# Kernel optimization log

Measured on AMD Instinct MI355X. Metric: run time of the kernel, lower is better.

## Reference

```python
import jax, jax.numpy as jnp
import numpy as np

HIDDEN = 256
ATOM_DIM = 133
BOND_DIM = 14
MOL_DIM = 200
N_ATOMS = 120000
N_BONDS = 240000
MAX_DEG = 6
N_MOL = 4096
DEPTH = 3
EPS = 1e-5
NEG_SLOPE = 0.01


def _leaky(x):
    return jnp.where(x >= 0, x, NEG_SLOPE * x)


def _bn(x, w, b):
    # BatchNorm1d in training mode: batch mean / biased batch variance
    mu = jnp.mean(x, axis=0)
    var = jnp.var(x, axis=0)
    return (x - mu) * jax.lax.rsqrt(var + EPS) * w + b


def setup_inputs() -> dict:
    key = jax.random.key(0)
    ks = jax.random.split(key, 12)
    s = 0.02
    return {
        "atom_features": jax.random.normal(ks[0], (N_ATOMS, ATOM_DIM), jnp.float32),
        "bond_features": jax.random.normal(ks[1], (N_BONDS, BOND_DIM), jnp.float32),
        "bond_index": jax.random.randint(ks[2], (2, N_BONDS), 0, N_ATOMS, jnp.int32),
        "molecule_features": jax.random.normal(ks[3], (N_MOL, MOL_DIM), jnp.float32),
        # 1-based bond ids; 0 means padding (maps to prepended zero row)
        "atom_incoming_bond_map": jax.random.randint(ks[4], (N_ATOMS, MAX_DEG), 0, N_BONDS + 1, jnp.int32),
        "bond_reverse_map": jax.random.randint(ks[5], (N_BONDS,), 0, N_BONDS, jnp.int32),
        "atom_to_mol": jnp.sort(jax.random.randint(ks[6], (N_ATOMS,), 0, N_MOL, jnp.int32)),
        "W_i_w": jax.random.normal(ks[7], (HIDDEN, ATOM_DIM + BOND_DIM), jnp.float32) * s,
        "W_i_b": jnp.zeros((HIDDEN,), jnp.float32),
        "W_m_w": jax.random.normal(ks[8], (HIDDEN, HIDDEN), jnp.float32) * s,
        "W_m_b": jnp.zeros((HIDDEN,), jnp.float32),
        "W_a_w": jax.random.normal(ks[9], (HIDDEN, ATOM_DIM + HIDDEN), jnp.float32) * s,
        "W_a_b": jnp.zeros((HIDDEN,), jnp.float32),
        "bn_w": jnp.ones((HIDDEN,), jnp.float32),
        "bn_b": jnp.zeros((HIDDEN,), jnp.float32),
    }


def _atom_incoming_sum(h, aibm):
    # padded_h[0] is the zero row; aibm holds 1-based bond indices (0 = pad)
    padded_h = jnp.concatenate([jnp.zeros((1, h.shape[1]), h.dtype), h], axis=0)
    return padded_h[aibm].sum(axis=1)  # [n_atoms, H]


def reference(atom_features, bond_features, bond_index, molecule_features,
              atom_incoming_bond_map, bond_reverse_map, atom_to_mol,
              W_i_w, W_i_b, W_m_w, W_m_b, W_a_w, W_a_b, bn_w, bn_b):
    src = bond_index[0]
    # initial bond hidden states
    x = jnp.concatenate([bond_features, atom_features[src]], axis=1)
    h0 = _bn(_leaky(x @ W_i_w.T + W_i_b), bn_w, bn_b)
    h = h0
    for _ in range(DEPTH):
        atom_sums = _atom_incoming_sum(h, atom_incoming_bond_map)
        # message for bond b (v->w): sum of incoming bonds at v minus reverse bond
        m = atom_sums[src] - h[bond_reverse_map]
        h = _bn(_leaky(h0 + m @ W_m_w.T + W_m_b), bn_w, bn_b)
        # dropout_prob = 0.0 -> identity
    # bond -> atom pooling (empty atoms yield the cached zero vector)
    m_v = _atom_incoming_sum(h, atom_incoming_bond_map)
    h_v = _bn(_leaky(jnp.concatenate([atom_features, m_v], axis=1) @ W_a_w.T + W_a_b), bn_w, bn_b)
    # atom -> molecule pooling
    h_mol = jax.ops.segment_sum(h_v, atom_to_mol, num_segments=molecule_features.shape[0])
    return jnp.concatenate([h_mol, molecule_features], axis=1)
```

## Files before the change

### kernel.cpp

```cpp
#include <hip/hip_runtime.h>
#include <hip/hip_bf16.h>
#include <stdint.h>

#define NBONDS 240000
#define NATOMS 120000
#define HID    256
#define ADIM   133
#define BDIM   14
#define MOLDIM 200
#define NMOL   4096
#define KI     160
#define KM     256
#define KA     416
#define OUTW   456
#define BN_EPS 1e-5f
#define SLOPE  0.01f

typedef unsigned short u16;
typedef unsigned int   u32;
typedef __attribute__((ext_vector_type(8))) short short8;
typedef __attribute__((ext_vector_type(4))) float f32x4;

__device__ __forceinline__ float bf2f(u16 b){
  u32 u = ((u32)b) << 16;
  return __builtin_bit_cast(float, u);
}
__device__ __forceinline__ u16 f2bf(float f){
  u32 u = __builtin_bit_cast(u32, f);
  u32 r = (u + 0x7FFFu + ((u >> 16) & 1u)) >> 16;
  return (u16)r;
}
__device__ __forceinline__ void gload16(const void* g, void* l){
  __builtin_amdgcn_global_load_lds((const __attribute__((address_space(1))) u32*)g,
                                   (__attribute__((address_space(3))) u32*)l, 16, 0, 0);
}
__device__ __forceinline__ float leaky(float v){ return v >= 0.f ? v : SLOPE*v; }

__global__ void zero_f(float* p, int n){
  int i = blockIdx.x*blockDim.x + threadIdx.x;
  if(i < n) p[i] = 0.f;
}
__global__ void diag_k(float* out, int n, float wsz){
  int i = blockIdx.x*blockDim.x + threadIdx.x;
  for(; i < n; i += gridDim.x*blockDim.x) out[i] = (i == 0) ? wsz : 0.f;
}

__global__ void cvt_weights(const float* wi, const float* wm, const float* wa,
                            u16* wib, u16* wmb, u16* wab){
  int idx = blockIdx.x*blockDim.x + threadIdx.x;
  const int T0 = 256*KI, T1 = T0 + 256*KM, T2 = T1 + 256*KA;
  for(; idx < T2; idx += gridDim.x*blockDim.x){
    if(idx < T0){
      int n = idx / KI, k = idx % KI;
      wib[idx] = f2bf(k < 147 ? wi[n*147+k] : 0.f);
    } else if(idx < T1){
      int j = idx - T0;
      wmb[j] = f2bf(wm[j]);
    } else {
      int j = idx - T1;
      int n = j / KA, k = j % KA;
      float v = 0.f;
      if(k < 256)      v = wa[n*389 + 133 + k];
      else if(k < 389) v = wa[n*389 + (k - 256)];
      wab[j] = f2bf(v);
    }
  }
}

__global__ void affine_k(const float* __restrict__ stats, float* __restrict__ aff,
                         float invN, const float* __restrict__ bnw, const float* __restrict__ bnb){
  int c = threadIdx.x;
  float mu  = stats[c] * invN;
  float var = stats[256+c]*invN - mu*mu;
  float rs  = rsqrtf(var + BN_EPS);
  float sc  = rs * bnw[c];
  aff[c]     = sc;
  aff[256+c] = bnb[c] - mu*sc;
}


__global__ __launch_bounds__(256) void gemm0_k(
    const float* __restrict__ bondf, const float* __restrict__ atomf,
    const int* __restrict__ bidx, const u16* __restrict__ wib,
    const float* __restrict__ bi_, u16* __restrict__ Hout,
    float* __restrict__ stats)
{
  __shared__ u16 lA[2][4][64][8];
  __shared__ u16 lB[2][4][256][8];
  __shared__ float sred[512];
  const int tid=threadIdx.x, wave=tid>>6, lane=tid&63;
  const int wm=wave>>1, wn=wave&1, l15=lane&15, l4=lane>>4;
  const int r=tid&63, c=tid>>6;
  const int row0=blockIdx.x*64, row=row0+r;
  const int src = bidx[row];

  f32x4 acc[2][8];
  #pragma unroll
  for(int i=0;i<2;i++)
    #pragma unroll
    for(int j=0;j<8;j++){ f32x4 z={0.f,0.f,0.f,0.f}; acc[i][j]=z; }

  auto stgB=[&](int buf,int ks){
    #pragma unroll
    for(int kc=0;kc<4;kc++)
      gload16(wib + (size_t)(wave*64+lane)*KI + ks*32 + kc*8, &lB[buf][kc][wave*64][0]);
  };
  auto stgA=[&](int buf,int ks){
    int k0 = ks*32 + c*8;
    short8 o;
    #pragma unroll
    for(int e=0;e<8;e++){
      int kg=k0+e; float x=0.f;
      if(kg<BDIM) x=bondf[row*BDIM+kg];
      else if(kg<BDIM+ADIM) x=atomf[(size_t)src*ADIM+kg-BDIM];
      o[e]=(short)f2bf(x);
    }
    *(short8*)&lA[buf][c][r][0]=o;
  };
  auto mm=[&](int cur){
    short8 af[2];
    #pragma unroll
    for(int mf=0;mf<2;mf++) af[mf]=*(const short8*)&lA[cur][l4][wm*32+mf*16+l15][0];
    #pragma unroll
    for(int nf=0;nf<8;nf++){
      short8 b8=*(const short8*)&lB[cur][l4][wn*128+nf*16+l15][0];
      #pragma unroll
      for(int mf=0;mf<2;mf++)
        acc[mf][nf]=__builtin_amdgcn_mfma_f32_16x16x32_bf16(af[mf],b8,acc[mf][nf],0,0,0);
    }
  };

  stgA(0,0); stgB(0,0);
  __syncthreads();
  #pragma unroll
  for(int ks=0;ks<5;ks++){
    int cur=ks&1;
    if(ks<4){ stgA(cur^1,ks+1); stgB(cur^1,ks+1); }
    mm(cur);
    __syncthreads();
  }
  sred[tid]=0.f; sred[256+tid]=0.f;
  __syncthreads();
  #pragma unroll
  for(int nf=0;nf<8;nf++){
    int col=wn*128+nf*16+l15;
    float bc=bi_[col], ps=0.f, pq=0.f;
    #pragma unroll
    for(int mf=0;mf<2;mf++)
      #pragma unroll
      for(int j=0;j<4;j++){
        int grow=row0+wm*32+mf*16+l4*4+j;
        float h=leaky(acc[mf][nf][j]+bc);
        Hout[(size_t)grow*HID+col]=f2bf(h);
        ps+=h; pq+=h*h;
      }
    atomicAdd(&sred[col],ps); atomicAdd(&sred[256+col],pq);
  }
  __syncthreads();
  atomicAdd(&stats[tid],sred[tid]); atomicAdd(&stats[256+tid],sred[256+tid]);
}

__global__ __launch_bounds__(256) void gemml_k(
    const float* __restrict__ bondf, const float* __restrict__ atomf,
    const int* __restrict__ bidx, const int* __restrict__ brm,
    const int* __restrict__ aibm, const u16* __restrict__ Hin,
    const u16* __restrict__ zrow, const u16* __restrict__ wmb,
    const float* __restrict__ bm_, const u16* __restrict__ wib,
    const float* __restrict__ bi_, const float* __restrict__ ain,
    const float* __restrict__ aff0, u16* __restrict__ Hout,
    float* __restrict__ stats)
{
  __shared__ u16 lA[2][4][64][8];
  __shared__ u16 lB[2][4][256][8];
  __shared__ float sred[512];
  const int tid=threadIdx.x, wave=tid>>6, lane=tid&63;
  const int wm=wave>>1, wn=wave&1, l15=lane&15, l4=lane>>4;
  const int r=tid&63, c=tid>>6;
  const int row0=blockIdx.x*64, row=row0+r;

  sred[tid]=ain[tid]; sred[256+tid]=ain[256+tid];

  const int src = bidx[row];
  const int rev = brm[row];
  const u16* gbase[7];
  int cnt=0;
  #pragma unroll
  for(int j=0;j<6;j++){
    int id = aibm[src*6+j];
    gbase[j] = (id>0) ? (Hin + (size_t)(id-1)*HID) : zrow;
    cnt += (id>0);
  }
  gbase[6] = Hin + (size_t)rev*HID;
  const float cntm1 = (float)(cnt-1);

  f32x4 acc[2][8];
  #pragma unroll
  for(int i=0;i<2;i++)
    #pragma unroll
    for(int j=0;j<8;j++){ f32x4 z={0.f,0.f,0.f,0.f}; acc[i][j]=z; }

  auto stgB=[&](int buf,int ks,const u16* W,int ldk){
    #pragma unroll
    for(int kc=0;kc<4;kc++)
      gload16(W + (size_t)(wave*64+lane)*ldk + ks*32 + kc*8, &lB[buf][kc][wave*64][0]);
  };
  auto stgA1=[&](int buf,int ks){
    int kofs = ks*32 + c*8;
    short8 v[7];
    #pragma unroll
    for(int j=0;j<7;j++) v[j]=*(const short8*)(gbase[j]+kofs);
    short8 o;
    #pragma unroll
    for(int e=0;e<8;e++){
      float s=0.f;
      #pragma unroll
      for(int j=0;j<6;j++) s+=bf2f((u16)v[j][e]);
      s-=bf2f((u16)v[6][e]);
      float mv = sred[kofs+e]*s + cntm1*sred[256+kofs+e];
      o[e]=(short)f2bf(mv);
    }
    *(short8*)&lA[buf][c][r][0]=o;
  };
  auto stgA0=[&](int buf,int ks){
    int k0 = ks*32 + c*8;
    short8 o;
    #pragma unroll
    for(int e=0;e<8;e++){
      int kg=k0+e; float x=0.f;
      if(kg<BDIM) x=bondf[row*BDIM+kg];
      else if(kg<BDIM+ADIM) x=atomf[(size_t)src*ADIM+kg-BDIM];
      o[e]=(short)f2bf(x);
    }
    *(short8*)&lA[buf][c][r][0]=o;
  };
  auto mm=[&](int cur){
    short8 af[2];
    #pragma unroll
    for(int mf=0;mf<2;mf++) af[mf]=*(const short8*)&lA[cur][l4][wm*32+mf*16+l15][0];
    #pragma unroll
    for(int nf=0;nf<8;nf++){
      short8 b8=*(const short8*)&lB[cur][l4][wn*128+nf*16+l15][0];
      #pragma unroll
      for(int mf=0;mf<2;mf++)
        acc[mf][nf]=__builtin_amdgcn_mfma_f32_16x16x32_bf16(af[mf],b8,acc[mf][nf],0,0,0);
    }
  };

  __syncthreads();
  stgA1(0,0); stgB(0,0,wmb,KM);
  __syncthreads();
  #pragma unroll
  for(int ks=0;ks<8;ks++){
    int cur=ks&1;
    if(ks<7){ stgA1(cur^1,ks+1); stgB(cur^1,ks+1,wmb,KM); }
    mm(cur);
    __syncthreads();
  }
  u32 p1[2][8][2];
  #pragma unroll
  for(int mf=0;mf<2;mf++)
    #pragma unroll
    for(int nf=0;nf<8;nf++){
      p1[mf][nf][0]=((u32)f2bf(acc[mf][nf][1])<<16)|f2bf(acc[mf][nf][0]);
      p1[mf][nf][1]=((u32)f2bf(acc[mf][nf][3])<<16)|f2bf(acc[mf][nf][2]);
      f32x4 z={0.f,0.f,0.f,0.f}; acc[mf][nf]=z;
    }

  stgA0(0,0); stgB(0,0,wib,KI);
  __syncthreads();
  #pragma unroll
  for(int ks=0;ks<5;ks++){
    int cur=ks&1;
    if(ks<4){ stgA0(cur^1,ks+1); stgB(cur^1,ks+1,wib,KI); }
    mm(cur);
    __syncthreads();
  }

  sred[tid]=0.f; sred[256+tid]=0.f;
  __syncthreads();
  #pragma unroll
  for(int nf=0;nf<8;nf++){
    int col=wn*128+nf*16+l15;
    float bic=bi_[col], bmc=bm_[col];
    float s0=aff0[col], t0=aff0[256+col];
    float ps=0.f,pq=0.f;
    #pragma unroll
    for(int mf=0;mf<2;mf++)
      #pragma unroll
      for(int j=0;j<4;j++){
        int grow=row0+wm*32+mf*16+l4*4+j;
        float v0 = leaky(acc[mf][nf][j]+bic);
        v0 = s0*v0 + t0;
        u32 pw = p1[mf][nf][j>>1];
        float u1 = bf2f((u16)((j&1) ? (pw>>16) : (pw&0xffff)));
        float h = leaky(v0 + u1 + bmc);
        Hout[(size_t)grow*HID+col]=f2bf(h);
        ps+=h; pq+=h*h;
      }
    atomicAdd(&sred[col],ps); atomicAdd(&sred[256+col],pq);
  }
  __syncthreads();
  atomicAdd(&stats[tid],sred[tid]); atomicAdd(&stats[256+tid],sred[256+tid]);
}

__global__ __launch_bounds__(256) void gemmf_k(
    const float* __restrict__ atomf, const int* __restrict__ aibm,
    const u16* __restrict__ Hin, const u16* __restrict__ zrow,
    const u16* __restrict__ wab, const float* __restrict__ ba_,
    const float* __restrict__ ain, u16* __restrict__ Hvout,
    float* __restrict__ stats)
{
  __shared__ u16 lA[2][4][64][8];
  __shared__ u16 lB[2][4][256][8];
  __shared__ float sred[512];
  const int tid=threadIdx.x, wave=tid>>6, lane=tid&63;
  const int wm=wave>>1, wn=wave&1, l15=lane&15, l4=lane>>4;
  const int r=tid&63, c=tid>>6;
  const int row0=blockIdx.x*64, row=row0+r;

  sred[tid]=ain[tid]; sred[256+tid]=ain[256+tid];

  const u16* gbase[6];
  int cnt=0;
  #pragma unroll
  for(int j=0;j<6;j++){
    int id = aibm[row*6+j];
    gbase[j] = (id>0) ? (Hin + (size_t)(id-1)*HID) : zrow;
    cnt += (id>0);
  }
  const float cntf = (float)cnt;

  f32x4 acc[2][8];
  #pragma unroll
  for(int i=0;i<2;i++)
    #pragma unroll
    for(int j=0;j<8;j++){ f32x4 z={0.f,0.f,0.f,0.f}; acc[i][j]=z; }

  auto stgB=[&](int buf,int ks){
    #pragma unroll
    for(int kc=0;kc<4;kc++)
      gload16(wab + (size_t)(wave*64+lane)*KA + ks*32 + kc*8, &lB[buf][kc][wave*64][0]);
  };
  auto stgA=[&](int buf,int ks){
    int k0 = ks*32 + c*8;
    short8 o;
    if(ks<8){
      short8 v[6];
      #pragma unroll
      for(int j=0;j<6;j++) v[j]=*(const short8*)(gbase[j]+k0);
      #pragma unroll
      for(int e=0;e<8;e++){
        float s=0.f;
        #pragma unroll
        for(int j=0;j<6;j++) s+=bf2f((u16)v[j][e]);
        float mv = sred[k0+e]*s + cntf*sred[256+k0+e];
        o[e]=(short)f2bf(mv);
      }
    } else {
      #pragma unroll
      for(int e=0;e<8;e++){
        int kg = k0 + e - 256;
        float x = (kg < ADIM) ? atomf[(size_t)row*ADIM + kg] : 0.f;
        o[e]=(short)f2bf(x);
      }
    }
    *(short8*)&lA[buf][c][r][0]=o;
  };
  auto mm=[&](int cur){
    short8 af[2];
    #pragma unroll
    for(int mf=0;mf<2;mf++) af[mf]=*(const short8*)&lA[cur][l4][wm*32+mf*16+l15][0];
    #pragma unroll
    for(int nf=0;nf<8;nf++){
      short8 b8=*(const short8*)&lB[cur][l4][wn*128+nf*16+l15][0];
      #pragma unroll
      for(int mf=0;mf<2;mf++)
        acc[mf][nf]=__builtin_amdgcn_mfma_f32_16x16x32_bf16(af[mf],b8,acc[mf][nf],0,0,0);
    }
  };

  __syncthreads();
  stgA(0,0); stgB(0,0);
  __syncthreads();
  #pragma unroll
  for(int ks=0;ks<13;ks++){
    int cur=ks&1;
    if(ks<12){ stgA(cur^1,ks+1); stgB(cur^1,ks+1); }
    mm(cur);
    __syncthreads();
  }
  sred[tid]=0.f; sred[256+tid]=0.f;
  __syncthreads();
  #pragma unroll
  for(int nf=0;nf<8;nf++){
    int col=wn*128+nf*16+l15;
    float bc=ba_[col], ps=0.f,pq=0.f;
    #pragma unroll
    for(int mf=0;mf<2;mf++)
      #pragma unroll
      for(int j=0;j<4;j++){
        int grow=row0+wm*32+mf*16+l4*4+j;
        float h=leaky(acc[mf][nf][j]+bc);
        Hvout[(size_t)grow*HID+col]=f2bf(h);
        ps+=h; pq+=h*h;
      }
    atomicAdd(&sred[col],ps); atomicAdd(&sred[256+col],pq);
  }
  __syncthreads();
  atomicAdd(&stats[tid],sred[tid]); atomicAdd(&stats[256+tid],sred[256+tid]);
}

__device__ __forceinline__ int lbound(const int* a, int n, int v){
  int lo = 0, hi = n;
  while(lo < hi){ int mid = (lo+hi) >> 1; if(a[mid] < v) lo = mid+1; else hi = mid; }
  return lo;
}

__global__ void pool_k(const u16* __restrict__ hv, const float* __restrict__ aff,
                       const int* __restrict__ a2m, const float* __restrict__ molf,
                       float* __restrict__ outp){
  int m = blockIdx.x;
  int t = threadIdx.x;
  int start = lbound(a2m, NATOMS, m);
  int end   = lbound(a2m, NATOMS, m+1);
  int rg = t >> 5, cg = t & 31;
  float s[8];
  #pragma unroll
  for(int j=0;j<8;j++) s[j] = 0.f;
  for(int a = start + rg; a < end; a += 8){
    short8 v = *(const short8*)(hv + (size_t)a*HID + cg*8);
    #pragma unroll
    for(int j=0;j<8;j++) s[j] += bf2f((u16)v[j]);
  }
  __shared__ float red[8][256];
  #pragma unroll
  for(int j=0;j<8;j++) red[rg][cg*8+j] = s[j];
  __syncthreads();
  if(t < 256){
    float S = 0.f;
    #pragma unroll
    for(int r=0;r<8;r++) S += red[r][t];
    float cnt = (float)(end - start);
    outp[(size_t)m*OUTW + t] = aff[t]*S + cnt*aff[256+t];
  }
  if(t < MOLDIM){
    outp[(size_t)m*OUTW + HID + t] = molf[(size_t)m*MOLDIM + t];
  }
}

extern "C" void kernel_launch(void* const* d_in, const int* in_sizes, int n_in,
                              void* d_out, int out_size, void* d_ws, size_t ws_size,
                              hipStream_t stream){
  const float* atomf = (const float*)d_in[0];
  const float* bondf = (const float*)d_in[1];
  const int*   bidx  = (const int*)  d_in[2];
  const float* molf  = (const float*)d_in[3];
  const int*   aibm  = (const int*)  d_in[4];
  const int*   brm   = (const int*)  d_in[5];
  const int*   a2m   = (const int*)  d_in[6];
  const float* wi    = (const float*)d_in[7];
  const float* bi    = (const float*)d_in[8];
  const float* wm    = (const float*)d_in[9];
  const float* bm    = (const float*)d_in[10];
  const float* wa    = (const float*)d_in[11];
  const float* ba    = (const float*)d_in[12];
  const float* bnw   = (const float*)d_in[13];
  const float* bnb   = (const float*)d_in[14];
  float* outp = (float*)d_out;

  char* wsp = (char*)d_ws;
  size_t off = 0;
  auto alloc = [&](size_t bytes)->void*{
    void* p = wsp + off; off += (bytes + 255) & ~(size_t)255; return p;
  };
  u16* HA   = (u16*)alloc((size_t)NBONDS*HID*2);
  u16* HB   = (u16*)alloc((size_t)NBONDS*HID*2);
  u16* wib  = (u16*)alloc((size_t)256*KI*2);
  u16* wmb  = (u16*)alloc((size_t)256*KM*2);
  u16* wab  = (u16*)alloc((size_t)256*KA*2);
  float* stats = (float*)alloc(5*512*sizeof(float));
  float* affn  = (float*)alloc(5*512*sizeof(float));
  float* zrowf = (float*)alloc(512);
  size_t need = off;

  if(ws_size < need){
    diag_k<<<1024, 256, 0, stream>>>(outp, out_size, (float)ws_size);
    return;
  }
  const u16* zrow = (const u16*)zrowf;

  zero_f<<<(5248+255)/256, 256, 0, stream>>>(stats, 5248);
  cvt_weights<<<416, 256, 0, stream>>>(wi, wm, wa, wib, wmb, wab);

  gemm0_k<<<NBONDS/64, 256, 0, stream>>>(bondf, atomf, bidx, wib, bi, HA, stats);
  affine_k<<<1, 256, 0, stream>>>(stats, affn, 1.f/NBONDS, bnw, bnb);

  for(int t=0; t<3; t++){
    const u16* Hin  = (t & 1) ? HB : HA;
    u16*       Hout = (t & 1) ? HA : HB;
    gemml_k<<<NBONDS/64, 256, 0, stream>>>(bondf, atomf, bidx, brm, aibm,
                                           Hin, zrow, wmb, bm, wib, bi,
                                           affn + t*512, affn, Hout,
                                           stats + (t+1)*512);
    affine_k<<<1, 256, 0, stream>>>(stats + (t+1)*512, affn + (t+1)*512,
                                    1.f/NBONDS, bnw, bnb);
  }

  gemmf_k<<<NATOMS/64, 256, 0, stream>>>(atomf, aibm, HB, zrow, wab, ba,
                                         affn + 3*512, HA, stats + 4*512);
  affine_k<<<1, 256, 0, stream>>>(stats + 4*512, affn + 4*512, 1.f/NATOMS, bnw, bnb);

  pool_k<<<NMOL, 256, 0, stream>>>(HA, affn + 4*512, a2m, molf, outp);
}
```

Baseline: 1.988 ms.

## Split message gather out of GEMM kernels into separate gather kernels

New measurement: 1.870 ms. 1.06x faster.

```diff
diff --git a/kernel.cpp b/kernel.cpp
--- a/kernel.cpp
+++ b/kernel.cpp
@@ -52,7 +52,10 @@
   for(; idx < T2; idx += gridDim.x*blockDim.x){
     if(idx < T0){
       int n = idx / KI, k = idx % KI;
-      wib[idx] = f2bf(k < 147 ? wi[n*147+k] : 0.f);
+      float v = 0.f;
+      if(k < 133)      v = wi[n*147 + 14 + k];
+      else if(k < 147) v = wi[n*147 + (k - 133)];
+      wib[idx] = f2bf(v);
     } else if(idx < T1){
       int j = idx - T0;
       wmb[j] = f2bf(wm[j]);
@@ -76,6 +79,75 @@
   float sc  = rs * bnw[c];
   aff[c]     = sc;
   aff[256+c] = bnb[c] - mu*sc;
+}
+
+__global__ __launch_bounds__(256) void msg_k(
+    const int* __restrict__ bidx, const int* __restrict__ brm,
+    const int* __restrict__ aibm, const u16* __restrict__ Hin,
+    const u16* __restrict__ zrow, const float* __restrict__ ain,
+    u16* __restrict__ Mout)
+{
+  int t = threadIdx.x;
+  int b = blockIdx.x*8 + (t>>5);
+  int lane = t & 31;
+  int src = bidx[b];
+  int rev = brm[b];
+  const u16* gb[7];
+  int cnt = 0;
+  #pragma unroll
+  for(int j=0;j<6;j++){
+    int id = aibm[src*6+j];
+    gb[j] = (id>0) ? (Hin + (size_t)(id-1)*HID) : zrow;
+    cnt += (id>0);
+  }
+  gb[6] = Hin + (size_t)rev*HID;
+  int c = lane*8;
+  short8 v[7];
+  #pragma unroll
+  for(int j=0;j<7;j++) v[j] = *(const short8*)(gb[j]+c);
+  float cm1 = (float)(cnt-1);
+  short8 o;
+  #pragma unroll
+  for(int e=0;e<8;e++){
+    float s = 0.f;
+    #pragma unroll
+    for(int j=0;j<6;j++) s += bf2f((u16)v[j][e]);
+    s -= bf2f((u16)v[6][e]);
+    o[e] = (short)f2bf(ain[c+e]*s + cm1*ain[256+c+e]);
+  }
+  *(short8*)(Mout + (size_t)b*HID + c) = o;
+}
+
+__global__ __launch_bounds__(256) void msgv_k(
+    const int* __restrict__ aibm, const u16* __restrict__ Hin,
+    const u16* __restrict__ zrow, const float* __restrict__ ain,
+    u16* __restrict__ Mv)
+{
+  int t = threadIdx.x;
+  int a = blockIdx.x*8 + (t>>5);
+  int lane = t & 31;
+  const u16* gb[6];
+  int cnt = 0;
+  #pragma unroll
+  for(int j=0;j<6;j++){
+    int id = aibm[a*6+j];
+    gb[j] = (id>0) ? (Hin + (size_t)(id-1)*HID) : zrow;
+    cnt += (id>0);
+  }
+  int c = lane*8;
+  short8 v[6];
+  #pragma unroll
+  for(int j=0;j<6;j++) v[j] = *(const short8*)(gb[j]+c);
+  float cf = (float)cnt;
+  short8 o;
+  #pragma unroll
+  for(int e=0;e<8;e++){
+    float s = 0.f;
+    #pragma unroll
+    for(int j=0;j<6;j++) s += bf2f((u16)v[j][e]);
+    o[e] = (short)f2bf(ain[c+e]*s + cf*ain[256+c+e]);
+  }
+  *(short8*)(Mv + (size_t)a*HID + c) = o;
 }
 
 
@@ -111,8 +183,8 @@
     #pragma unroll
     for(int e=0;e<8;e++){
       int kg=k0+e; float x=0.f;
-      if(kg<BDIM) x=bondf[row*BDIM+kg];
-      else if(kg<BDIM+ADIM) x=atomf[(size_t)src*ADIM+kg-BDIM];
+      if(kg<ADIM) x=atomf[(size_t)src*ADIM+kg];
+      else if(kg<ADIM+BDIM) x=bondf[(size_t)row*BDIM+kg-ADIM];
       o[e]=(short)f2bf(x);
     }
     *(short8*)&lA[buf][c][r][0]=o;
@@ -162,12 +234,118 @@
 
 __global__ __launch_bounds__(256) void gemml_k(
     const float* __restrict__ bondf, const float* __restrict__ atomf,
-    const int* __restrict__ bidx, const int* __restrict__ brm,
-    const int* __restrict__ aibm, const u16* __restrict__ Hin,
-    const u16* __restrict__ zrow, const u16* __restrict__ wmb,
-    const float* __restrict__ bm_, const u16* __restrict__ wib,
-    const float* __restrict__ bi_, const float* __restrict__ ain,
-    const float* __restrict__ aff0, u16* __restrict__ Hout,
+    const int* __restrict__ bidx, u16* __restrict__ Mh,
+    const u16* __restrict__ wmb, const float* __restrict__ bm_,
+    const u16* __restrict__ wib, const float* __restrict__ bi_,
+    const float* __restrict__ aff0, float* __restrict__ stats)
+{
+  __shared__ u16 lA[2][4][64][8];
+  __shared__ u16 lB[2][4][256][8];
+  __shared__ float sred[512];
+  const int tid=threadIdx.x, wave=tid>>6, lane=tid&63;
+  const int wm=wave>>1, wn=wave&1, l15=lane&15, l4=lane>>4;
+  const int r=tid&63, c=tid>>6;
+  const int row0=blockIdx.x*64, row=row0+r;
+  const int src = bidx[row];
+
+  f32x4 acc[2][8];
+  #pragma unroll
+  for(int i=0;i<2;i++)
+    #pragma unroll
+    for(int j=0;j<8;j++){ f32x4 z={0.f,0.f,0.f,0.f}; acc[i][j]=z; }
+
+  auto stgB=[&](int buf,int ks,const u16* W,int ldk){
+    #pragma unroll
+    for(int kc=0;kc<4;kc++)
+      gload16(W + (size_t)(wave*64+lane)*ldk + ks*32 + kc*8, &lB[buf][kc][wave*64][0]);
+  };
+  auto stgA1=[&](int buf,int ks){
+    gload16(Mh + (size_t)(row0+lane)*KM + ks*32 + wave*8, &lA[buf][wave][0][0]);
+  };
+  auto stgA0=[&](int buf,int ks){
+    int k0 = ks*32 + c*8;
+    short8 o;
+    #pragma unroll
+    for(int e=0;e<8;e++){
+      int kg=k0+e; float x=0.f;
+      if(kg<ADIM) x=atomf[(size_t)src*ADIM+kg];
+      else if(kg<ADIM+BDIM) x=bondf[(size_t)row*BDIM+kg-ADIM];
+      o[e]=(short)f2bf(x);
+    }
+    *(short8*)&lA[buf][c][r][0]=o;
+  };
+  auto mm=[&](int cur){
+    short8 af[2];
+    #pragma unroll
+    for(int mf=0;mf<2;mf++) af[mf]=*(const short8*)&lA[cur][l4][wm*32+mf*16+l15][0];
+    #pragma unroll
+    for(int nf=0;nf<8;nf++){
+      short8 b8=*(const short8*)&lB[cur][l4][wn*128+nf*16+l15][0];
+      #pragma unroll
+      for(int mf=0;mf<2;mf++)
+        acc[mf][nf]=__builtin_amdgcn_mfma_f32_16x16x32_bf16(af[mf],b8,acc[mf][nf],0,0,0);
+    }
+  };
+
+  stgA1(0,0); stgB(0,0,wmb,KM);
+  __syncthreads();
+  #pragma unroll
+  for(int ks=0;ks<8;ks++){
+    int cur=ks&1;
+    if(ks<7){ stgA1(cur^1,ks+1); stgB(cur^1,ks+1,wmb,KM); }
+    mm(cur);
+    __syncthreads();
+  }
+  u32 p1[2][8][2];
+  #pragma unroll
+  for(int mf=0;mf<2;mf++)
+    #pragma unroll
+    for(int nf=0;nf<8;nf++){
+      p1[mf][nf][0]=((u32)f2bf(acc[mf][nf][1])<<16)|f2bf(acc[mf][nf][0]);
+      p1[mf][nf][1]=((u32)f2bf(acc[mf][nf][3])<<16)|f2bf(acc[mf][nf][2]);
+      f32x4 z={0.f,0.f,0.f,0.f}; acc[mf][nf]=z;
+    }
+
+  stgA0(0,0); stgB(0,0,wib,KI);
+  __syncthreads();
+  #pragma unroll
+  for(int ks=0;ks<5;ks++){
+    int cur=ks&1;
+    if(ks<4){ stgA0(cur^1,ks+1); stgB(cur^1,ks+1,wib,KI); }
+    mm(cur);
+    __syncthreads();
+  }
+
+  sred[tid]=0.f; sred[256+tid]=0.f;
+  __syncthreads();
+  #pragma unroll
+  for(int nf=0;nf<8;nf++){
+    int col=wn*128+nf*16+l15;
+    float bic=bi_[col], bmc=bm_[col];
+    float s0=aff0[col], t0=aff0[256+col];
+    float ps=0.f,pq=0.f;
+    #pragma unroll
+    for(int mf=0;mf<2;mf++)
+      #pragma unroll
+      for(int j=0;j<4;j++){
+        int grow=row0+wm*32+mf*16+l4*4+j;
+        float v0 = leaky(acc[mf][nf][j]+bic);
+        v0 = s0*v0 + t0;
+        u32 pw = p1[mf][nf][j>>1];
+        float u1 = bf2f((u16)((j&1) ? (pw>>16) : (pw&0xffff)));
+        float h = leaky(v0 + u1 + bmc);
+        Mh[(size_t)grow*HID+col]=f2bf(h);
+        ps+=h; pq+=h*h;
+      }
+    atomicAdd(&sred[col],ps); atomicAdd(&sred[256+col],pq);
+  }
+  __syncthreads();
+  atomicAdd(&stats[tid],sred[tid]); atomicAdd(&stats[256+tid],sred[256+tid]);
+}
+
+__global__ __launch_bounds__(256) void gemmf_k(
+    const float* __restrict__ atomf, u16* __restrict__ Mv,
+    const u16* __restrict__ wab, const float* __restrict__ ba_,
     float* __restrict__ stats)
 {
   __shared__ u16 lA[2][4][64][8];
@@ -178,158 +356,6 @@
   const int r=tid&63, c=tid>>6;
   const int row0=blockIdx.x*64, row=row0+r;
 
-  sred[tid]=ain[tid]; sred[256+tid]=ain[256+tid];
-
-  const int src = bidx[row];
-  const int rev = brm[row];
-  const u16* gbase[7];
-  int cnt=0;
-  #pragma unroll
-  for(int j=0;j<6;j++){
-    int id = aibm[src*6+j];
-    gbase[j] = (id>0) ? (Hin + (size_t)(id-1)*HID) : zrow;
-    cnt += (id>0);
-  }
-  gbase[6] = Hin + (size_t)rev*HID;
-  const float cntm1 = (float)(cnt-1);
-
-  f32x4 acc[2][8];
-  #pragma unroll
-  for(int i=0;i<2;i++)
-    #pragma unroll
-    for(int j=0;j<8;j++){ f32x4 z={0.f,0.f,0.f,0.f}; acc[i][j]=z; }
-
-  auto stgB=[&](int buf,int ks,const u16* W,int ldk){
-    #pragma unroll
-    for(int kc=0;kc<4;kc++)
-      gload16(W + (size_t)(wave*64+lane)*ldk + ks*32 + kc*8, &lB[buf][kc][wave*64][0]);
-  };
-  auto stgA1=[&](int buf,int ks){
-    int kofs = ks*32 + c*8;
-    short8 v[7];
-    #pragma unroll
-    for(int j=0;j<7;j++) v[j]=*(const short8*)(gbase[j]+kofs);
-    short8 o;
-    #pragma unroll
-    for(int e=0;e<8;e++){
-      float s=0.f;
-      #pragma unroll
-      for(int j=0;j<6;j++) s+=bf2f((u16)v[j][e]);
-      s-=bf2f((u16)v[6][e]);
-      float mv = sred[kofs+e]*s + cntm1*sred[256+kofs+e];
-      o[e]=(short)f2bf(mv);
-    }
-    *(short8*)&lA[buf][c][r][0]=o;
-  };
-  auto stgA0=[&](int buf,int ks){
-    int k0 = ks*32 + c*8;
-    short8 o;
-    #pragma unroll
-    for(int e=0;e<8;e++){
-      int kg=k0+e; float x=0.f;
-      if(kg<BDIM) x=bondf[row*BDIM+kg];
-      else if(kg<BDIM+ADIM) x=atomf[(size_t)src*ADIM+kg-BDIM];
-      o[e]=(short)f2bf(x);
-    }
-    *(short8*)&lA[buf][c][r][0]=o;
-  };
-  auto mm=[&](int cur){
-    short8 af[2];
-    #pragma unroll
-    for(int mf=0;mf<2;mf++) af[mf]=*(const short8*)&lA[cur][l4][wm*32+mf*16+l15][0];
-    #pragma unroll
-    for(int nf=0;nf<8;nf++){
-      short8 b8=*(const short8*)&lB[cur][l4][wn*128+nf*16+l15][0];
-      #pragma unroll
-      for(int mf=0;mf<2;mf++)
-        acc[mf][nf]=__builtin_amdgcn_mfma_f32_16x16x32_bf16(af[mf],b8,acc[mf][nf],0,0,0);
-    }
-  };
-
-  __syncthreads();
-  stgA1(0,0); stgB(0,0,wmb,KM);
-  __syncthreads();
-  #pragma unroll
-  for(int ks=0;ks<8;ks++){
-    int cur=ks&1;
-    if(ks<7){ stgA1(cur^1,ks+1); stgB(cur^1,ks+1,wmb,KM); }
-    mm(cur);
-    __syncthreads();
-  }
-  u32 p1[2][8][2];
-  #pragma unroll
-  for(int mf=0;mf<2;mf++)
-    #pragma unroll
-    for(int nf=0;nf<8;nf++){
-      p1[mf][nf][0]=((u32)f2bf(acc[mf][nf][1])<<16)|f2bf(acc[mf][nf][0]);
-      p1[mf][nf][1]=((u32)f2bf(acc[mf][nf][3])<<16)|f2bf(acc[mf][nf][2]);
-      f32x4 z={0.f,0.f,0.f,0.f}; acc[mf][nf]=z;
-    }
-
-  stgA0(0,0); stgB(0,0,wib,KI);
-  __syncthreads();
-  #pragma unroll
-  for(int ks=0;ks<5;ks++){
-    int cur=ks&1;
-    if(ks<4){ stgA0(cur^1,ks+1); stgB(cur^1,ks+1,wib,KI); }
-    mm(cur);
-    __syncthreads();
-  }
-
-  sred[tid]=0.f; sred[256+tid]=0.f;
-  __syncthreads();
-  #pragma unroll
-  for(int nf=0;nf<8;nf++){
-    int col=wn*128+nf*16+l15;
-    float bic=bi_[col], bmc=bm_[col];
-    float s0=aff0[col], t0=aff0[256+col];
-    float ps=0.f,pq=0.f;
-    #pragma unroll
-    for(int mf=0;mf<2;mf++)
-      #pragma unroll
-      for(int j=0;j<4;j++){
-        int grow=row0+wm*32+mf*16+l4*4+j;
-        float v0 = leaky(acc[mf][nf][j]+bic);
-        v0 = s0*v0 + t0;
-        u32 pw = p1[mf][nf][j>>1];
-        float u1 = bf2f((u16)((j&1) ? (pw>>16) : (pw&0xffff)));
-        float h = leaky(v0 + u1 + bmc);
-        Hout[(size_t)grow*HID+col]=f2bf(h);
-        ps+=h; pq+=h*h;
-      }
-    atomicAdd(&sred[col],ps); atomicAdd(&sred[256+col],pq);
-  }
-  __syncthreads();
-  atomicAdd(&stats[tid],sred[tid]); atomicAdd(&stats[256+tid],sred[256+tid]);
-}
-
-__global__ __launch_bounds__(256) void gemmf_k(
-    const float* __restrict__ atomf, const int* __restrict__ aibm,
-    const u16* __restrict__ Hin, const u16* __restrict__ zrow,
-    const u16* __restrict__ wab, const float* __restrict__ ba_,
-    const float* __restrict__ ain, u16* __restrict__ Hvout,
-    float* __restrict__ stats)
-{
-  __shared__ u16 lA[2][4][64][8];
-  __shared__ u16 lB[2][4][256][8];
-  __shared__ float sred[512];
-  const int tid=threadIdx.x, wave=tid>>6, lane=tid&63;
-  const int wm=wave>>1, wn=wave&1, l15=lane&15, l4=lane>>4;
-  const int r=tid&63, c=tid>>6;
-  const int row0=blockIdx.x*64, row=row0+r;
-
-  sred[tid]=ain[tid]; sred[256+tid]=ain[256+tid];
-
-  const u16* gbase[6];
-  int cnt=0;
-  #pragma unroll
-  for(int j=0;j<6;j++){
-    int id = aibm[row*6+j];
-    gbase[j] = (id>0) ? (Hin + (size_t)(id-1)*HID) : zrow;
-    cnt += (id>0);
-  }
-  const float cntf = (float)cnt;
-
   f32x4 acc[2][8];
   #pragma unroll
   for(int i=0;i<2;i++)
@@ -342,29 +368,19 @@
       gload16(wab + (size_t)(wave*64+lane)*KA + ks*32 + kc*8, &lB[buf][kc][wave*64][0]);
   };
   auto stgA=[&](int buf,int ks){
-    int k0 = ks*32 + c*8;
-    short8 o;
     if(ks<8){
-      short8 v[6];
-      #pragma unroll
-      for(int j=0;j<6;j++) v[j]=*(const short8*)(gbase[j]+k0);
+      gload16(Mv + (size_t)(row0+lane)*KM + ks*32 + wave*8, &lA[buf][wave][0][0]);
+    } else {
+      int k0 = ks*32 + c*8 - 256;
+      short8 o;
       #pragma unroll
       for(int e=0;e<8;e++){
-        float s=0.f;
-        #pragma unroll
-        for(int j=0;j<6;j++) s+=bf2f((u16)v[j][e]);
-        float mv = sred[k0+e]*s + cntf*sred[256+k0+e];
-        o[e]=(short)f2bf(mv);
-      }
-    } else {
-      #pragma unroll
-      for(int e=0;e<8;e++){
-        int kg = k0 + e - 256;
+        int kg = k0 + e;
         float x = (kg < ADIM) ? atomf[(size_t)row*ADIM + kg] : 0.f;
         o[e]=(short)f2bf(x);
       }
-    }
-    *(short8*)&lA[buf][c][r][0]=o;
+      *(short8*)&lA[buf][c][r][0]=o;
+    }
   };
   auto mm=[&](int cur){
     short8 af[2];
@@ -379,7 +395,6 @@
     }
   };
 
-  __syncthreads();
   stgA(0,0); stgB(0,0);
   __syncthreads();
   #pragma unroll
@@ -401,7 +416,7 @@
       for(int j=0;j<4;j++){
         int grow=row0+wm*32+mf*16+l4*4+j;
         float h=leaky(acc[mf][nf][j]+bc);
-        Hvout[(size_t)grow*HID+col]=f2bf(h);
+        Mv[(size_t)grow*HID+col]=f2bf(h);
         ps+=h; pq+=h*h;
       }
     atomicAdd(&sred[col],ps); atomicAdd(&sred[256+col],pq);
@@ -496,18 +511,19 @@
   affine_k<<<1, 256, 0, stream>>>(stats, affn, 1.f/NBONDS, bnw, bnb);
 
   for(int t=0; t<3; t++){
-    const u16* Hin  = (t & 1) ? HB : HA;
-    u16*       Hout = (t & 1) ? HA : HB;
-    gemml_k<<<NBONDS/64, 256, 0, stream>>>(bondf, atomf, bidx, brm, aibm,
-                                           Hin, zrow, wmb, bm, wib, bi,
-                                           affn + t*512, affn, Hout,
+    const u16* Hin = (t & 1) ? HB : HA;
+    u16*       Hm  = (t & 1) ? HA : HB;
+    msg_k<<<NBONDS/8, 256, 0, stream>>>(bidx, brm, aibm, Hin, zrow,
+                                        affn + t*512, Hm);
+    gemml_k<<<NBONDS/64, 256, 0, stream>>>(bondf, atomf, bidx, Hm,
+                                           wmb, bm, wib, bi, affn,
                                            stats + (t+1)*512);
     affine_k<<<1, 256, 0, stream>>>(stats + (t+1)*512, affn + (t+1)*512,
                                     1.f/NBONDS, bnw, bnb);
   }
 
-  gemmf_k<<<NATOMS/64, 256, 0, stream>>>(atomf, aibm, HB, zrow, wab, ba,
-                                         affn + 3*512, HA, stats + 4*512);
+  msgv_k<<<NATOMS/8, 256, 0, stream>>>(aibm, HB, zrow, affn + 3*512, HA);
+  gemmf_k<<<NATOMS/64, 256, 0, stream>>>(atomf, HA, wab, ba, stats + 4*512);
   affine_k<<<1, 256, 0, stream>>>(stats + 4*512, affn + 4*512, 1.f/NATOMS, bnw, bnb);
 
   pool_k<<<NMOL, 256, 0, stream>>>(HA, affn + 4*512, a2m, molf, outp);
```
